# Optimization experiments

Measured on AMD Instinct MI355X. Metric: run time of the kernel, lower is better.

## Reference

```python
import jax, jax.numpy as jnp
import numpy as np

N_NODES = 100000
N_EDGES = 1600000
IN_SIZE = 512
HID_SIZE = 256
OUT_SIZE = 16
DROP_P = 0.5


def _degrees(idx, n):
    d = jax.ops.segment_sum(jnp.ones(idx.shape[0], jnp.float32), idx, num_segments=n)
    return jnp.maximum(d, 1.0)  # DGL clamps zero degrees to 1


def graph_conv(src, dst, feat, W, b, activation=None):
    # DGL GraphConv, norm='both': D_in^{-1/2} A D_out^{-1/2} X W + b
    n = feat.shape[0]
    inv_sqrt_dout = _degrees(src, n) ** -0.5   # out-degree of source nodes
    inv_sqrt_din = _degrees(dst, n) ** -0.5    # in-degree of destination nodes
    h = feat * inv_sqrt_dout[:, None]
    h = h @ W  # in_feats >= out_feats -> transform before aggregation (same math)
    # message passing: scatter-add source messages to destinations
    h = jax.ops.segment_sum(h[src], dst, num_segments=n)
    h = h * inv_sqrt_din[:, None] + b
    if activation is not None:
        h = activation(h)
    return h


def setup_inputs() -> dict:
    key = jax.random.key(0)
    ks = jax.random.split(key, 9)
    features = jax.random.normal(ks[0], (N_NODES, IN_SIZE), jnp.float32)
    src = jax.random.randint(ks[1], (N_EDGES,), 0, N_NODES)
    dst = jax.random.randint(ks[2], (N_EDGES,), 0, N_NODES)
    W1 = jax.random.normal(ks[3], (IN_SIZE, HID_SIZE), jnp.float32) / np.sqrt(IN_SIZE).astype(np.float32)
    b1 = jnp.zeros((HID_SIZE,), jnp.float32)
    W2 = jax.random.normal(ks[4], (HID_SIZE, HID_SIZE), jnp.float32) / np.sqrt(HID_SIZE).astype(np.float32)
    b2 = jnp.zeros((HID_SIZE,), jnp.float32)
    W3 = jax.random.normal(ks[5], (HID_SIZE, OUT_SIZE), jnp.float32) / np.sqrt(HID_SIZE).astype(np.float32)
    b3 = jnp.zeros((OUT_SIZE,), jnp.float32)
    return {"features": features, "src": src, "dst": dst,
            "W1": W1, "b1": b1, "W2": W2, "b2": b2, "W3": W3, "b3": b3}


def reference(features, src, dst, W1, b1, W2, b2, W3, b3):
    # layer 0: GraphConv + relu
    h = graph_conv(src, dst, features, W1, b1, activation=jax.nn.relu)
    # dropout(0.5) before layer 1 (deterministic fixed-key mask, training semantics)
    keep = jax.random.bernoulli(jax.random.key(42), 1.0 - DROP_P, h.shape)
    h = jnp.where(keep, h / (1.0 - DROP_P), 0.0)
    # layer 1: GraphConv (no activation)
    h = graph_conv(src, dst, h, W2, b2, activation=None)
    # layer 2: plain Linear head
    return h @ W3 + b3
```

## Files before the change

kernel.cpp:

```cpp
#include <hip/hip_runtime.h>
#include <stdint.h>

#define NN    100000
#define NE    1600000
#define IN_F  512
#define HID   256
#define OUTF  16
#define NPAD  100096
#define NBK   391
#define EPB   8192

typedef unsigned int u32;
typedef __bf16 bfrag  __attribute__((ext_vector_type(8)));
typedef float  f32x4  __attribute__((ext_vector_type(4)));
typedef short  s16x8  __attribute__((ext_vector_type(8)));

__device__ __forceinline__ u32 rotl32(u32 x, int r){ return (x<<r)|(x>>(32-r)); }

__device__ __forceinline__ bool drop_keep(u32 i){
    const u32 ks0 = 0u, ks1 = 42u, ks2 = 0x1BD11BDAu ^ 0u ^ 42u;
    u32 x0 = 0u + ks0;
    u32 x1 = i  + ks1;
#define TFR(r) { x0 += x1; x1 = rotl32(x1,(r)); x1 ^= x0; }
    TFR(13) TFR(15) TFR(26) TFR(6)   x0 += ks1; x1 += ks2 + 1u;
    TFR(17) TFR(29) TFR(16) TFR(24)  x0 += ks2; x1 += ks0 + 2u;
    TFR(13) TFR(15) TFR(26) TFR(6)   x0 += ks0; x1 += ks1 + 3u;
    TFR(17) TFR(29) TFR(16) TFR(24)  x0 += ks1; x1 += ks2 + 4u;
    TFR(13) TFR(15) TFR(26) TFR(6)   x0 += ks2; x1 += ks0 + 5u;
#undef TFR
    return ((x0 ^ x1) >> 31) == 0u;
}

__device__ __forceinline__ short f2b(float f){
    union { float f; u32 u; } v; v.f = f;
    u32 r = (v.u + 0x7FFFu + ((v.u >> 16) & 1u)) >> 16;
    return (short)r;
}
__device__ __forceinline__ float blo(u32 u){ union{u32 u; float f;} v; v.u = u << 16;         return v.f; }
__device__ __forceinline__ float bhi(u32 u){ union{u32 u; float f;} v; v.u = u & 0xFFFF0000u; return v.f; }

__device__ __forceinline__ u32 cvt_pk_bf16(float lo, float hi){
    u32 r;
    asm("v_cvt_pk_bf16_f32 %0, %1, %2" : "=v"(r) : "v"(lo), "v"(hi));
    return r;
}

__device__ __forceinline__ void gll16(const void* g, void* l){
    __builtin_amdgcn_global_load_lds((const __attribute__((address_space(1))) void*)g,
                                     (__attribute__((address_space(3))) void*)l, 16, 0, 0);
}


__global__ __launch_bounds__(256) void build_hist(const int4* __restrict__ src4,
                                                  const int4* __restrict__ dst4,
                                                  int* deg_out, int* __restrict__ bcnt){
    __shared__ int h[NBK];
    int t = threadIdx.x;
    for (int i = t; i < NBK; i += 256) h[i] = 0;
    __syncthreads();
    for (int i = blockIdx.x * 256 + t; i < NE / 4; i += gridDim.x * 256) {
        int4 s = src4[i];
        int4 d = dst4[i];
        atomicAdd(&deg_out[s.x], 1);
        atomicAdd(&deg_out[s.y], 1);
        atomicAdd(&deg_out[s.z], 1);
        atomicAdd(&deg_out[s.w], 1);
        atomicAdd(&h[d.x >> 8], 1);
        atomicAdd(&h[d.y >> 8], 1);
        atomicAdd(&h[d.z >> 8], 1);
        atomicAdd(&h[d.w >> 8], 1);
    }
    __syncthreads();
    for (int i = t; i < NBK; i += 256)
        if (h[i]) atomicAdd(&bcnt[i], h[i]);
}

__global__ __launch_bounds__(256) void finalize_deg(const int* __restrict__ deg_out,
                                                    const int* __restrict__ row_ptr,
                                                    float* isdo, float* isdi){
    int i = blockIdx.x * blockDim.x + threadIdx.x;
    if (i < NN) {
        isdo[i] = rsqrtf(fmaxf((float)deg_out[i], 1.0f));
        isdi[i] = rsqrtf(fmaxf((float)(row_ptr[i + 1] - row_ptr[i]), 1.0f));
    }
}

__global__ __launch_bounds__(512) void bucket_scan(const int* __restrict__ bcnt,
                                                   int* __restrict__ bbase,
                                                   int* __restrict__ bcur,
                                                   int* __restrict__ row_ptr){
    __shared__ int sh[512];
    int t = threadIdx.x;
    int v = (t < NBK) ? bcnt[t] : 0;
    sh[t] = v;
    __syncthreads();
    for (int off = 1; off < 512; off <<= 1) {
        int a = (t >= off) ? sh[t - off] : 0;
        __syncthreads();
        sh[t] += a;
        __syncthreads();
    }
    int excl = sh[t] - v;
    if (t < NBK) { bbase[t] = excl; bcur[t] = excl; }
    if (t == 0)  { bbase[NBK] = NE; row_ptr[NN] = NE; }
}

__global__ __launch_bounds__(256) void bucket_scatter(const int* __restrict__ src,
                                                      const int* __restrict__ dst,
                                                      int* bcur, u32* __restrict__ tmp){
    __shared__ int lh[NBK];
    __shared__ int lb[NBK];
    int t = threadIdx.x;
    for (int i = t; i < NBK; i += 256) lh[i] = 0;
    __syncthreads();
    const int e0 = blockIdx.x * EPB;
    for (int k = t * 4; k < EPB; k += 1024) {
        int e = e0 + k;
        if (e < NE) {
            int4 d = *(const int4*)(dst + e);
            atomicAdd(&lh[d.x >> 8], 1);
            atomicAdd(&lh[d.y >> 8], 1);
            atomicAdd(&lh[d.z >> 8], 1);
            atomicAdd(&lh[d.w >> 8], 1);
        }
    }
    __syncthreads();
    for (int i = t; i < NBK; i += 256) {
        int c = lh[i];
        if (c) lb[i] = atomicAdd(&bcur[i], c);
        lh[i] = 0;
    }
    __syncthreads();
    for (int k = t * 4; k < EPB; k += 1024) {
        int e = e0 + k;
        if (e < NE) {
            int4 d = *(const int4*)(dst + e);
            int4 s = *(const int4*)(src + e);
            int b0 = d.x >> 8, b1 = d.y >> 8, b2 = d.z >> 8, b3 = d.w >> 8;
            int r0 = atomicAdd(&lh[b0], 1);
            tmp[lb[b0] + r0] = ((u32)s.x << 8) | ((u32)d.x & 255u);
            int r1 = atomicAdd(&lh[b1], 1);
            tmp[lb[b1] + r1] = ((u32)s.y << 8) | ((u32)d.y & 255u);
            int r2 = atomicAdd(&lh[b2], 1);
            tmp[lb[b2] + r2] = ((u32)s.z << 8) | ((u32)d.z & 255u);
            int r3 = atomicAdd(&lh[b3], 1);
            tmp[lb[b3] + r3] = ((u32)s.w << 8) | ((u32)d.w & 255u);
        }
    }
}

__global__ __launch_bounds__(256) void bucket_finalize(const u32* __restrict__ tmp,
                                                       const int* __restrict__ bbase,
                                                       int* __restrict__ row_ptr,
                                                       int* __restrict__ col_src){
    __shared__ int h[256];
    __shared__ int wtot[4];
    const int t = threadIdx.x;
    const int b = blockIdx.x;
    const int base = bbase[b];
    const int cnt  = bbase[b + 1] - base;
    h[t] = 0;
    __syncthreads();
    for (int k = t; k < cnt; k += 256)
        atomicAdd(&h[tmp[base + k] & 255u], 1);
    __syncthreads();
    int v = h[t];
    int lane = t & 63, w = t >> 6;
    int s = v;
    #pragma unroll
    for (int off = 1; off < 64; off <<= 1) {
        int u = __shfl_up(s, off);
        if (lane >= off) s += u;
    }
    if (lane == 63) wtot[w] = s;
    __syncthreads();
    int woff = 0;
    #pragma unroll
    for (int i = 0; i < 4; ++i) woff += (i < w) ? wtot[i] : 0;
    int excl = woff + s - v;
    int d = (b << 8) + t;
    if (d < NN) row_ptr[d] = base + excl;
    h[t] = excl;
    __syncthreads();
    for (int k = t; k < cnt; k += 256) {
        u32 p = tmp[base + k];
        int r = atomicAdd(&h[p & 255u], 1);
        col_src[base + r] = (int)(p >> 8);
    }
}


template<int Kd, int Nd>
__global__ __launch_bounds__(256) void convert_wt(const float* __restrict__ W,
                                                  short* __restrict__ WT){
    int i = blockIdx.x * 256 + threadIdx.x;
    if (i >= Kd * Nd) return;
    int n = i / Kd, k = i - n * Kd;
    WT[i] = f2b(W[(size_t)k * Nd + n]);
}

__global__ __launch_bounds__(256) void gemm_x(const float* __restrict__ X,
                                              const short* __restrict__ BT,
                                              const float* __restrict__ isdo,
                                              short* __restrict__ C){
    __shared__ __align__(16) float As[2 * 4160];
    __shared__ __align__(16) short Bs[2 * 8320];

    const int t = threadIdx.x;
    const int wave = t >> 6, lane = t & 63;
    const int bm = blockIdx.x * 128;

    const float* paA[4];
    #pragma unroll
    for (int g = 0; g < 4; ++g) {
        int row = bm + wave * 32 + g * 8 + (lane >> 3);
        if (row > NN - 1) row = NN - 1;
        paA[g] = X + (size_t)row * IN_F + (lane & 7) * 4;
    }
    const short* paB[4];
    #pragma unroll
    for (int g = 0; g < 4; ++g) {
        int col = (wave * 4 + g) * 16 + (lane >> 2);
        paB[g] = BT + (size_t)col * IN_F + (lane & 3) * 8;
    }

    const int wr = (wave >> 1) * 64;
    const int wc = (wave & 1) * 128;
    const int kq = lane >> 4, r15 = lane & 15;

    f32x4 acc[4][8];
    #pragma unroll
    for (int m = 0; m < 4; ++m)
        #pragma unroll
        for (int n = 0; n < 8; ++n) acc[m][n] = (f32x4)0.0f;

#define STAGE_X(BUF, K0) { \
    float* dA = As + (BUF) * 4160 + wave * 1040; \
    gll16(paA[0] + (K0), dA);       gll16(paA[1] + (K0), dA + 260); \
    gll16(paA[2] + (K0), dA + 520); gll16(paA[3] + (K0), dA + 780); \
    short* dB = Bs + (BUF) * 8320 + wave * 2080; \
    gll16(paB[0] + (K0), dB);        gll16(paB[1] + (K0), dB + 520); \
    gll16(paB[2] + (K0), dB + 1040); gll16(paB[3] + (K0), dB + 1560); }

#define COMPUTE_X(BUF) { \
    const float* AsC = As + (BUF) * 4160; \
    const short* BsC = Bs + (BUF) * 8320; \
    bfrag af[4], bfg[8]; \
    _Pragma("unroll") \
    for (int m = 0; m < 4; ++m) { \
        int r  = wr + m * 16 + r15; \
        const float* ap = AsC + (r >> 3) * 260 + (r & 7) * 32 + kq * 8; \
        float4 f0 = *(const float4*)ap; \
        float4 f1 = *(const float4*)(ap + 4); \
        uint4 q = make_uint4(cvt_pk_bf16(f0.x, f0.y), cvt_pk_bf16(f0.z, f0.w), \
                             cvt_pk_bf16(f1.x, f1.y), cvt_pk_bf16(f1.z, f1.w)); \
        af[m] = *(bfrag*)&q; \
    } \
    _Pragma("unroll") \
    for (int n = 0; n < 8; ++n) { \
        int cg = (wc >> 4) + n; \
        bfg[n] = *(const bfrag*)(BsC + cg * 520 + r15 * 32 + kq * 8); \
    } \
    _Pragma("unroll") \
    for (int m = 0; m < 4; ++m) \
        _Pragma("unroll") \
        for (int n = 0; n < 8; ++n) \
            acc[m][n] = __builtin_amdgcn_mfma_f32_16x16x32_bf16(af[m], bfg[n], acc[m][n], 0, 0, 0); }

    const int NT = IN_F / 32;
    STAGE_X(0, 0);
    int cur = 0;
    for (int tt = 0; tt < NT - 1; ++tt) {
        STAGE_X(cur ^ 1, (tt + 1) * 32);
        asm volatile("s_waitcnt vmcnt(8)" ::: "memory");
        __builtin_amdgcn_s_barrier();
        COMPUTE_X(cur);
        asm volatile("" ::: "memory");
        __builtin_amdgcn_s_barrier();
        cur ^= 1;
    }
    asm volatile("s_waitcnt vmcnt(0)" ::: "memory");
    __builtin_amdgcn_s_barrier();
    COMPUTE_X(cur);
#undef STAGE_X
#undef COMPUTE_X

    const int crow0 = bm + wr + (lane >> 4) * 4;
    const int ccol0 = wc + r15;
    #pragma unroll
    for (int m = 0; m < 4; ++m)
        #pragma unroll
        for (int r = 0; r < 4; ++r) {
            int row = crow0 + m * 16 + r;
            float sc = (row < NN) ? isdo[row] : 0.0f;
            #pragma unroll
            for (int n = 0; n < 8; ++n)
                C[(size_t)row * HID + ccol0 + n * 16] = f2b(acc[m][n][r] * sc);
        }
}

template<int K>
__global__ __launch_bounds__(256) void gemm_bt(const short* __restrict__ A,
                                               const short* __restrict__ BT,
                                               short* __restrict__ C){
    __shared__ __align__(16) short As[2 * 4160];
    __shared__ __align__(16) short Bs[2 * 8320];

    const int t = threadIdx.x;
    const int wave = t >> 6, lane = t & 63;
    const int bm = blockIdx.x * 128;

    const short* paA[2];
    #pragma unroll
    for (int g = 0; g < 2; ++g) {
        int row = bm + (wave * 2 + g) * 16 + (lane >> 2);
        paA[g] = A + (size_t)row * K + (lane & 3) * 8;
    }
    const short* paB[4];
    #pragma unroll
    for (int g = 0; g < 4; ++g) {
        int col = (wave * 4 + g) * 16 + (lane >> 2);
        paB[g] = BT + (size_t)col * K + (lane & 3) * 8;
    }

    const int wr = (wave >> 1) * 64;
    const int wc = (wave & 1) * 128;
    const int kq = lane >> 4, r15 = lane & 15;

    f32x4 acc[4][8];
    #pragma unroll
    for (int m = 0; m < 4; ++m)
        #pragma unroll
        for (int n = 0; n < 8; ++n) acc[m][n] = (f32x4)0.0f;

#define STAGE_B(BUF, K0) { \
    short* dA = As + (BUF) * 4160 + wave * 1040; \
    gll16(paA[0] + (K0), dA); gll16(paA[1] + (K0), dA + 520); \
    short* dB = Bs + (BUF) * 8320 + wave * 2080; \
    gll16(paB[0] + (K0), dB);        gll16(paB[1] + (K0), dB + 520); \
    gll16(paB[2] + (K0), dB + 1040); gll16(paB[3] + (K0), dB + 1560); }

#define COMPUTE_B(BUF) { \
    const short* AsC = As + (BUF) * 4160; \
    const short* BsC = Bs + (BUF) * 8320; \
    bfrag af[4], bfg[8]; \
    _Pragma("unroll") \
    for (int m = 0; m < 4; ++m) { \
        int ch = (wr + m * 16) >> 4; \
        af[m] = *(const bfrag*)(AsC + ch * 520 + r15 * 32 + kq * 8); \
    } \
    _Pragma("unroll") \
    for (int n = 0; n < 8; ++n) { \
        int cg = (wc >> 4) + n; \
        bfg[n] = *(const bfrag*)(BsC + cg * 520 + r15 * 32 + kq * 8); \
    } \
    _Pragma("unroll") \
    for (int m = 0; m < 4; ++m) \
        _Pragma("unroll") \
        for (int n = 0; n < 8; ++n) \
            acc[m][n] = __builtin_amdgcn_mfma_f32_16x16x32_bf16(af[m], bfg[n], acc[m][n], 0, 0, 0); }

    const int NT = K / 32;
    STAGE_B(0, 0);
    int cur = 0;
    for (int tt = 0; tt < NT - 1; ++tt) {
        STAGE_B(cur ^ 1, (tt + 1) * 32);
        asm volatile("s_waitcnt vmcnt(6)" ::: "memory");
        __builtin_amdgcn_s_barrier();
        COMPUTE_B(cur);
        asm volatile("" ::: "memory");
        __builtin_amdgcn_s_barrier();
        cur ^= 1;
    }
    asm volatile("s_waitcnt vmcnt(0)" ::: "memory");
    __builtin_amdgcn_s_barrier();
    COMPUTE_B(cur);
#undef STAGE_B
#undef COMPUTE_B

    const int crow0 = bm + wr + (lane >> 4) * 4;
    const int ccol0 = wc + r15;
    #pragma unroll
    for (int m = 0; m < 4; ++m)
        #pragma unroll
        for (int n = 0; n < 8; ++n)
            #pragma unroll
            for (int r = 0; r < 4; ++r)
                C[(size_t)(crow0 + m * 16 + r) * HID + ccol0 + n * 16] = f2b(acc[m][n][r]);
}

template<int MODE>
__global__ __launch_bounds__(256) void gather_agg(const short* __restrict__ H,
                                                  const int* __restrict__ rp,
                                                  const int* __restrict__ cs,
                                                  const float* __restrict__ isdi,
                                                  const float* __restrict__ isdo,
                                                  const float* __restrict__ bias,
                                                  short* __restrict__ out){
    const int lane = threadIdx.x & 63;
    const int node = __builtin_amdgcn_readfirstlane((int)(blockIdx.x * 4) + (int)(threadIdx.x >> 6));
    const int e0  = rp[node];
    const int end = rp[node + 1];
    const int sub = lane & 31, half = lane >> 5;
    const u32 off16 = (u32)sub * 16u;
    const char* Hb = (const char*)H;

    float a[8] = {0,0,0,0,0,0,0,0};
    float b[8] = {0,0,0,0,0,0,0,0};

#define LD4(s) (*(const uint4*)(Hb + ((((u32)(s)) << 9) | off16)))
#define ACC(A, u) { A[0]+=blo(u.x); A[1]+=bhi(u.x); A[2]+=blo(u.y); A[3]+=bhi(u.y); \
                    A[4]+=blo(u.z); A[5]+=bhi(u.z); A[6]+=blo(u.w); A[7]+=bhi(u.w); }

    int eb = e0;
    for (; eb + 16 <= end; eb += 16) {
        int t0 = cs[eb+0],  t1 = cs[eb+1],  t2 = cs[eb+2],  t3 = cs[eb+3];
        int t4 = cs[eb+4],  t5 = cs[eb+5],  t6 = cs[eb+6],  t7 = cs[eb+7];
        int t8 = cs[eb+8],  t9 = cs[eb+9],  tA = cs[eb+10], tB = cs[eb+11];
        int tC = cs[eb+12], tD = cs[eb+13], tE = cs[eb+14], tF = cs[eb+15];
        int s0 = half ? t1 : t0;
        int s1 = half ? t3 : t2;
        int s2 = half ? t5 : t4;
        int s3 = half ? t7 : t6;
        int s4 = half ? t9 : t8;
        int s5 = half ? tB : tA;
        int s6 = half ? tD : tC;
        int s7 = half ? tF : tE;
        uint4 u0 = LD4(s0), u1 = LD4(s1), u2 = LD4(s2), u3 = LD4(s3);
        uint4 u4 = LD4(s4), u5 = LD4(s5), u6 = LD4(s6), u7 = LD4(s7);
        ACC(a, u0); ACC(b, u1); ACC(a, u2); ACC(b, u3);
        ACC(a, u4); ACC(b, u5); ACC(a, u6); ACC(b, u7);
    }
    for (; eb + 8 <= end; eb += 8) {
        int t0 = cs[eb+0], t1 = cs[eb+1], t2 = cs[eb+2], t3 = cs[eb+3];
        int t4 = cs[eb+4], t5 = cs[eb+5], t6 = cs[eb+6], t7 = cs[eb+7];
        int s0 = half ? t1 : t0;
        int s1 = half ? t3 : t2;
        int s2 = half ? t5 : t4;
        int s3 = half ? t7 : t6;
        uint4 u0 = LD4(s0), u1 = LD4(s1), u2 = LD4(s2), u3 = LD4(s3);
        ACC(a, u0); ACC(b, u1); ACC(a, u2); ACC(b, u3);
    }
    for (; eb + 2 <= end; eb += 2) {
        int t0 = cs[eb], t1 = cs[eb+1];
        int s = half ? t1 : t0;
        uint4 u = LD4(s);
        ACC(a, u);
    }
    if (eb < end) {
        int s = cs[eb];
        uint4 u = LD4(s);
        if (half == 0) { ACC(a, u); }
    }
#undef ACC
#undef LD4
    #pragma unroll
    for (int j = 0; j < 8; ++j) a[j] += b[j];

    const int srcl = lane >> 1;
    const bool oddq = (lane & 1) != 0;
    float v[4];
    #pragma unroll
    for (int j = 0; j < 4; ++j) {
        float p0 = __shfl(a[j],     srcl);
        float p1 = __shfl(a[j + 4], srcl);
        float q0 = __shfl(a[j],     srcl + 32);
        float q1 = __shfl(a[j + 4], srcl + 32);
        v[j] = oddq ? (p1 + q1) : (p0 + q0);
    }

    float sd = isdi[node];
    float4 bb = *(const float4*)(bias + lane * 4);
    float h0 = v[0] * sd + bb.x;
    float h1 = v[1] * sd + bb.y;
    float h2 = v[2] * sd + bb.z;
    float h3 = v[3] * sd + bb.w;

    if (MODE == 0) {
        float so2 = 2.0f * isdo[node];
        u32 base = (u32)node * HID + (u32)lane * 4;
        h0 = drop_keep(base + 0) ? fmaxf(h0, 0.f) * so2 : 0.f;
        h1 = drop_keep(base + 1) ? fmaxf(h1, 0.f) * so2 : 0.f;
        h2 = drop_keep(base + 2) ? fmaxf(h2, 0.f) * so2 : 0.f;
        h3 = drop_keep(base + 3) ? fmaxf(h3, 0.f) * so2 : 0.f;
    }

    uint2 wv;
    wv.x = ((u32)(unsigned short)f2b(h1) << 16) | (u32)(unsigned short)f2b(h0);
    wv.y = ((u32)(unsigned short)f2b(h3) << 16) | (u32)(unsigned short)f2b(h2);
    *(uint2*)((char*)out + (size_t)node * 512 + (u32)lane * 8u) = wv;
}

__global__ __launch_bounds__(256) void head_kernel(const short* __restrict__ H2,
                                                   const float* __restrict__ W3,
                                                   const float* __restrict__ b3,
                                                   float* __restrict__ out){
    __shared__ float W3s[HID * OUTF];
    __shared__ short rows[16][HID + 8];
    int t = threadIdx.x;
    for (int i = t; i < HID * OUTF; i += 256) W3s[i] = W3[i];
    const int n0 = blockIdx.x * 16;
    for (int c = t; c < 16 * 32; c += 256) {
        int r = c >> 5, cc = c & 31;
        *(s16x8*)(&rows[r][cc * 8]) = *(const s16x8*)(H2 + (size_t)(n0 + r) * HID + cc * 8);
    }
    __syncthreads();
    int nl = t >> 4, k = t & 15;
    float acc = 0.0f;
    #pragma unroll 4
    for (int j = 0; j < HID; ++j)
        acc += blo((u32)(unsigned short)rows[nl][j]) * W3s[j * OUTF + k];
    out[(size_t)(n0 + nl) * OUTF + k] = acc + b3[k];
}

extern "C" void kernel_launch(void* const* d_in, const int* in_sizes, int n_in,
                              void* d_out, int out_size, void* d_ws, size_t ws_size,
                              hipStream_t stream) {
    const float* X   = (const float*)d_in[0];
    const int*   src = (const int*)  d_in[1];
    const int*   dst = (const int*)  d_in[2];
    const float* W1  = (const float*)d_in[3];
    const float* b1  = (const float*)d_in[4];
    const float* W2  = (const float*)d_in[5];
    const float* b2  = (const float*)d_in[6];
    const float* W3  = (const float*)d_in[7];
    const float* b3  = (const float*)d_in[8];
    float* out = (float*)d_out;

    char* ws = (char*)d_ws;
    size_t o = 0;
    int*   deg_out = (int*)  (ws + o); o += (size_t)NN * 4;
    int*   bcnt    = (int*)  (ws + o); o += (size_t)NBK * 4;
    float* isdo    = (float*)(ws + o); o += (size_t)NN * 4;
    float* isdi    = (float*)(ws + o); o += (size_t)NN * 4;
    int*   row_ptr = (int*)  (ws + o); o += (size_t)(NN + 1) * 4;
    int*   bbase   = (int*)  (ws + o); o += (size_t)(NBK + 1) * 4;
    int*   bcur    = (int*)  (ws + o); o += (size_t)NBK * 4;
    int*   col_src = (int*)  (ws + o); o += (size_t)NE * 4;
    o = (o + 255) & ~(size_t)255;
    short* W1t = (short*)(ws + o); o += (size_t)IN_F * HID * 2;
    short* W2t = (short*)(ws + o); o += (size_t)HID * HID * 2;
    o = (o + 255) & ~(size_t)255;
    short* hA    = (short*)(ws + o); o += (size_t)NPAD * HID * 2;
    short* hB    = (short*)(ws + o); o += (size_t)NPAD * HID * 2;
    short* h2pre = (short*)(ws + o); o += (size_t)NPAD * HID * 2;
    if (ws_size < o) return;
    short* h2  = hA;
    u32*   tmp = (u32*)hB;

    const size_t zlen = (size_t)NN * 4 + (size_t)NBK * 4;
    hipMemsetAsync(deg_out, 0, zlen, stream);

    build_hist<<<256, 256, 0, stream>>>((const int4*)src, (const int4*)dst, deg_out, bcnt);
    bucket_scan<<<1, 512, 0, stream>>>(bcnt, bbase, bcur, row_ptr);
    bucket_scatter<<<(NE + EPB - 1) / EPB, 256, 0, stream>>>(src, dst, bcur, tmp);
    bucket_finalize<<<NBK, 256, 0, stream>>>(tmp, bbase, row_ptr, col_src);
    finalize_deg<<<(NN + 255) / 256, 256, 0, stream>>>(deg_out, row_ptr, isdo, isdi);

    convert_wt<IN_F, HID><<<IN_F * HID / 256, 256, 0, stream>>>(W1, W1t);
    convert_wt<HID, HID><<<HID * HID / 256, 256, 0, stream>>>(W2, W2t);

    gemm_x<<<NPAD / 128, 256, 0, stream>>>(X, W1t, isdo, hA);
    gather_agg<0><<<NN / 4, 256, 0, stream>>>(hA, row_ptr, col_src, isdi, isdo, b1, hB);

    gemm_bt<HID><<<NPAD / 128, 256, 0, stream>>>(hB, W2t, h2pre);
    gather_agg<1><<<NN / 4, 256, 0, stream>>>(h2pre, row_ptr, col_src, isdi, isdo, b2, h2);

    head_kernel<<<NN / 16, 256, 0, stream>>>(h2, W3, b3, out);
}
```

Before: 487.0 us.

## Restage GEMM LDS layout, predicate SpMM tail, and read head rows directly

The GEMM kernels now stage A and B tiles in LDS in an MFMA-fragment-major layout, with no padding and with a remapped global-to-LDS load pattern. This is meant to cut LDS bank conflicts and wasted space when fragments are read. The aggregation kernel replaces its serial 8/2/1 remainder loops with one predicated 16-edge batch that clamps indices and zeroes unused loads, trading a few extra loads for more memory parallelism. The head kernel drops its shared-memory row staging and reads bf16 rows straight from global memory as uint4, unpacking 8 values per load.

```diff
diff --git a/kernel.cpp b/kernel.cpp
--- a/kernel.cpp
+++ b/kernel.cpp
@@ -203,8 +203,8 @@
                                               const short* __restrict__ BT,
                                               const float* __restrict__ isdo,
                                               short* __restrict__ C){
-    __shared__ __align__(16) float As[2 * 4160];
-    __shared__ __align__(16) short Bs[2 * 8320];
+    __shared__ __align__(16) float As[2 * 4096];
+    __shared__ __align__(16) short Bs[2 * 8192];
 
     const int t = threadIdx.x;
     const int wave = t >> 6, lane = t & 63;
@@ -213,15 +213,17 @@
     const float* paA[4];
     #pragma unroll
     for (int g = 0; g < 4; ++g) {
-        int row = bm + wave * 32 + g * 8 + (lane >> 3);
+        int rg = wave * 2 + (g >> 1);
+        int q2 = g & 1;
+        int row = bm + rg * 16 + (lane & 15);
         if (row > NN - 1) row = NN - 1;
-        paA[g] = X + (size_t)row * IN_F + (lane & 7) * 4;
+        paA[g] = X + (size_t)row * IN_F + q2 * 16 + (lane >> 5) * 8 + ((lane >> 4) & 1) * 4;
     }
     const short* paB[4];
     #pragma unroll
     for (int g = 0; g < 4; ++g) {
-        int col = (wave * 4 + g) * 16 + (lane >> 2);
-        paB[g] = BT + (size_t)col * IN_F + (lane & 3) * 8;
+        int col = (wave * 4 + g) * 16 + (lane & 15);
+        paB[g] = BT + (size_t)col * IN_F + (lane >> 4) * 8;
     }
 
     const int wr = (wave >> 1) * 64;
@@ -235,23 +237,23 @@
         for (int n = 0; n < 8; ++n) acc[m][n] = (f32x4)0.0f;
 
 #define STAGE_X(BUF, K0) { \
-    float* dA = As + (BUF) * 4160 + wave * 1040; \
-    gll16(paA[0] + (K0), dA);       gll16(paA[1] + (K0), dA + 260); \
-    gll16(paA[2] + (K0), dA + 520); gll16(paA[3] + (K0), dA + 780); \
-    short* dB = Bs + (BUF) * 8320 + wave * 2080; \
-    gll16(paB[0] + (K0), dB);        gll16(paB[1] + (K0), dB + 520); \
-    gll16(paB[2] + (K0), dB + 1040); gll16(paB[3] + (K0), dB + 1560); }
+    float* dA = As + (BUF) * 4096 + wave * 1024; \
+    gll16(paA[0] + (K0), dA);       gll16(paA[1] + (K0), dA + 256); \
+    gll16(paA[2] + (K0), dA + 512); gll16(paA[3] + (K0), dA + 768); \
+    short* dB = Bs + (BUF) * 8192 + wave * 2048; \
+    gll16(paB[0] + (K0), dB);        gll16(paB[1] + (K0), dB + 512); \
+    gll16(paB[2] + (K0), dB + 1024); gll16(paB[3] + (K0), dB + 1536); }
 
 #define COMPUTE_X(BUF) { \
-    const float* AsC = As + (BUF) * 4160; \
-    const short* BsC = Bs + (BUF) * 8320; \
+    const float* AsC = As + (BUF) * 4096; \
+    const short* BsC = Bs + (BUF) * 8192; \
     bfrag af[4], bfg[8]; \
     _Pragma("unroll") \
     for (int m = 0; m < 4; ++m) { \
-        int r  = wr + m * 16 + r15; \
-        const float* ap = AsC + (r >> 3) * 260 + (r & 7) * 32 + kq * 8; \
+        int rg = (wr >> 4) + m; \
+        const float* ap = AsC + rg * 512 + kq * 128 + r15 * 4; \
         float4 f0 = *(const float4*)ap; \
-        float4 f1 = *(const float4*)(ap + 4); \
+        float4 f1 = *(const float4*)(ap + 64); \
         uint4 q = make_uint4(cvt_pk_bf16(f0.x, f0.y), cvt_pk_bf16(f0.z, f0.w), \
                              cvt_pk_bf16(f1.x, f1.y), cvt_pk_bf16(f1.z, f1.w)); \
         af[m] = *(bfrag*)&q; \
@@ -259,7 +261,7 @@
     _Pragma("unroll") \
     for (int n = 0; n < 8; ++n) { \
         int cg = (wc >> 4) + n; \
-        bfg[n] = *(const bfrag*)(BsC + cg * 520 + r15 * 32 + kq * 8); \
+        bfg[n] = *(const bfrag*)(BsC + cg * 512 + kq * 128 + r15 * 8); \
     } \
     _Pragma("unroll") \
     for (int m = 0; m < 4; ++m) \
@@ -303,8 +305,8 @@
 __global__ __launch_bounds__(256) void gemm_bt(const short* __restrict__ A,
                                                const short* __restrict__ BT,
                                                short* __restrict__ C){
-    __shared__ __align__(16) short As[2 * 4160];
-    __shared__ __align__(16) short Bs[2 * 8320];
+    __shared__ __align__(16) short As[2 * 4096];
+    __shared__ __align__(16) short Bs[2 * 8192];
 
     const int t = threadIdx.x;
     const int wave = t >> 6, lane = t & 63;
@@ -313,14 +315,14 @@
     const short* paA[2];
     #pragma unroll
     for (int g = 0; g < 2; ++g) {
-        int row = bm + (wave * 2 + g) * 16 + (lane >> 2);
-        paA[g] = A + (size_t)row * K + (lane & 3) * 8;
+        int row = bm + (wave * 2 + g) * 16 + (lane & 15);
+        paA[g] = A + (size_t)row * K + (lane >> 4) * 8;
     }
     const short* paB[4];
     #pragma unroll
     for (int g = 0; g < 4; ++g) {
-        int col = (wave * 4 + g) * 16 + (lane >> 2);
-        paB[g] = BT + (size_t)col * K + (lane & 3) * 8;
+        int col = (wave * 4 + g) * 16 + (lane & 15);
+        paB[g] = BT + (size_t)col * K + (lane >> 4) * 8;
     }
 
     const int wr = (wave >> 1) * 64;
@@ -334,25 +336,25 @@
         for (int n = 0; n < 8; ++n) acc[m][n] = (f32x4)0.0f;
 
 #define STAGE_B(BUF, K0) { \
-    short* dA = As + (BUF) * 4160 + wave * 1040; \
-    gll16(paA[0] + (K0), dA); gll16(paA[1] + (K0), dA + 520); \
-    short* dB = Bs + (BUF) * 8320 + wave * 2080; \
-    gll16(paB[0] + (K0), dB);        gll16(paB[1] + (K0), dB + 520); \
-    gll16(paB[2] + (K0), dB + 1040); gll16(paB[3] + (K0), dB + 1560); }
+    short* dA = As + (BUF) * 4096 + wave * 1024; \
+    gll16(paA[0] + (K0), dA); gll16(paA[1] + (K0), dA + 512); \
+    short* dB = Bs + (BUF) * 8192 + wave * 2048; \
+    gll16(paB[0] + (K0), dB);        gll16(paB[1] + (K0), dB + 512); \
+    gll16(paB[2] + (K0), dB + 1024); gll16(paB[3] + (K0), dB + 1536); }
 
 #define COMPUTE_B(BUF) { \
-    const short* AsC = As + (BUF) * 4160; \
-    const short* BsC = Bs + (BUF) * 8320; \
+    const short* AsC = As + (BUF) * 4096; \
+    const short* BsC = Bs + (BUF) * 8192; \
     bfrag af[4], bfg[8]; \
     _Pragma("unroll") \
     for (int m = 0; m < 4; ++m) { \
-        int ch = (wr + m * 16) >> 4; \
-        af[m] = *(const bfrag*)(AsC + ch * 520 + r15 * 32 + kq * 8); \
+        int rg = (wr >> 4) + m; \
+        af[m] = *(const bfrag*)(AsC + rg * 512 + kq * 128 + r15 * 8); \
     } \
     _Pragma("unroll") \
     for (int n = 0; n < 8; ++n) { \
         int cg = (wc >> 4) + n; \
-        bfg[n] = *(const bfrag*)(BsC + cg * 520 + r15 * 32 + kq * 8); \
+        bfg[n] = *(const bfrag*)(BsC + cg * 512 + kq * 128 + r15 * 8); \
     } \
     _Pragma("unroll") \
     for (int m = 0; m < 4; ++m) \
@@ -431,26 +433,36 @@
         ACC(a, u0); ACC(b, u1); ACC(a, u2); ACC(b, u3);
         ACC(a, u4); ACC(b, u5); ACC(a, u6); ACC(b, u7);
     }
-    for (; eb + 8 <= end; eb += 8) {
-        int t0 = cs[eb+0], t1 = cs[eb+1], t2 = cs[eb+2], t3 = cs[eb+3];
-        int t4 = cs[eb+4], t5 = cs[eb+5], t6 = cs[eb+6], t7 = cs[eb+7];
+    if (eb < end) {
+        const int last = end - 1;
+#define CSC(k) cs[(eb + (k) < end) ? (eb + (k)) : last]
+        int t0 = CSC(0),  t1 = CSC(1),  t2 = CSC(2),  t3 = CSC(3);
+        int t4 = CSC(4),  t5 = CSC(5),  t6 = CSC(6),  t7 = CSC(7);
+        int t8 = CSC(8),  t9 = CSC(9),  tA = CSC(10), tB = CSC(11);
+        int tC = CSC(12), tD = CSC(13), tE = CSC(14), tF = CSC(15);
+#undef CSC
         int s0 = half ? t1 : t0;
         int s1 = half ? t3 : t2;
         int s2 = half ? t5 : t4;
         int s3 = half ? t7 : t6;
+        int s4 = half ? t9 : t8;
+        int s5 = half ? tB : tA;
+        int s6 = half ? tD : tC;
+        int s7 = half ? tF : tE;
         uint4 u0 = LD4(s0), u1 = LD4(s1), u2 = LD4(s2), u3 = LD4(s3);
+        uint4 u4 = LD4(s4), u5 = LD4(s5), u6 = LD4(s6), u7 = LD4(s7);
+        const int lim = end - eb - half;
+        const uint4 z = make_uint4(0u, 0u, 0u, 0u);
+        u0 = ( 0 < lim) ? u0 : z;
+        u1 = ( 2 < lim) ? u1 : z;
+        u2 = ( 4 < lim) ? u2 : z;
+        u3 = ( 6 < lim) ? u3 : z;
+        u4 = ( 8 < lim) ? u4 : z;
+        u5 = (10 < lim) ? u5 : z;
+        u6 = (12 < lim) ? u6 : z;
+        u7 = (14 < lim) ? u7 : z;
         ACC(a, u0); ACC(b, u1); ACC(a, u2); ACC(b, u3);
-    }
-    for (; eb + 2 <= end; eb += 2) {
-        int t0 = cs[eb], t1 = cs[eb+1];
-        int s = half ? t1 : t0;
-        uint4 u = LD4(s);
-        ACC(a, u);
-    }
-    if (eb < end) {
-        int s = cs[eb];
-        uint4 u = LD4(s);
-        if (half == 0) { ACC(a, u); }
+        ACC(a, u4); ACC(b, u5); ACC(a, u6); ACC(b, u7);
     }
 #undef ACC
 #undef LD4
@@ -496,21 +508,23 @@
                                                    const float* __restrict__ b3,
                                                    float* __restrict__ out){
     __shared__ float W3s[HID * OUTF];
-    __shared__ short rows[16][HID + 8];
     int t = threadIdx.x;
     for (int i = t; i < HID * OUTF; i += 256) W3s[i] = W3[i];
-    const int n0 = blockIdx.x * 16;
-    for (int c = t; c < 16 * 32; c += 256) {
-        int r = c >> 5, cc = c & 31;
-        *(s16x8*)(&rows[r][cc * 8]) = *(const s16x8*)(H2 + (size_t)(n0 + r) * HID + cc * 8);
-    }
     __syncthreads();
     int nl = t >> 4, k = t & 15;
+    int n = blockIdx.x * 16 + nl;
+    const uint4* row = (const uint4*)(H2 + (size_t)n * HID);
     float acc = 0.0f;
     #pragma unroll 4
-    for (int j = 0; j < HID; ++j)
-        acc += blo((u32)(unsigned short)rows[nl][j]) * W3s[j * OUTF + k];
-    out[(size_t)(n0 + nl) * OUTF + k] = acc + b3[k];
+    for (int c = 0; c < 32; ++c) {
+        uint4 u = row[c];
+        const float* w = W3s + c * 8 * OUTF + k;
+        acc += blo(u.x) * w[0*OUTF] + bhi(u.x) * w[1*OUTF]
+             + blo(u.y) * w[2*OUTF] + bhi(u.y) * w[3*OUTF]
+             + blo(u.z) * w[4*OUTF] + bhi(u.z) * w[5*OUTF]
+             + blo(u.w) * w[6*OUTF] + bhi(u.w) * w[7*OUTF];
+    }
+    out[(size_t)n * OUTF + k] = acc + b3[k];
 }
 
 extern "C" void kernel_launch(void* const* d_in, const int* in_sizes, int n_in,
```

New measurement: 974.0 us. +100.0%, slower.
